# Kernel optimization log

Measured on AMD Instinct MI355X. Metric: run time of the kernel, lower is better.

The kernel has to match this reference:

```python
import jax, jax.numpy as jnp
import numpy as np

EPS_BN = 1e-5
NUM_DIR = 32


def _bn(x, g, b, m, v):
    # x: (B, C, N); inference-mode batchnorm over channel dim
    return (x - m[None, :, None]) / jnp.sqrt(v[None, :, None] + EPS_BN) * g[None, :, None] + b[None, :, None]


def _conv1(w, x):
    # 1x1 Conv1d: w (O, C), x (B, C, N) -> (B, O, N)
    return jnp.einsum('oc,bcn->bon', w, x)


def _knn_max(fc, idx):
    # fc: (B, C, N), idx: (B, N, K) -> max over gathered neighbors, (B, C, N)
    B = fc.shape[0]
    f_bnc = jnp.transpose(fc, (0, 2, 1))                      # (B, N, C)
    g = f_bnc[jnp.arange(B)[:, None, None], idx]              # (B, N, K, C)
    return jnp.transpose(g.max(axis=2), (0, 2, 1))            # (B, C, N)


def setup_inputs() -> dict:
    key = jax.random.key(0)
    ks = jax.random.split(key, 24)
    B, C, N, K = 4, 128, 8192, 16
    H = C // 2
    inp = {
        'f': jax.random.normal(ks[0], (B, C, N), jnp.float32),
        'dp': jax.random.normal(ks[1], (B, 3, N, K), jnp.float32),
        'qidx': jax.random.randint(ks[2], (B, N, K), 0, N),
        # DirectionalEncoding params
        'dir_vectors': jax.random.normal(ks[3], (NUM_DIR, 3), jnp.float32),
        'de_w1': jax.random.normal(ks[4], (H, NUM_DIR), jnp.float32) * 0.1,
        'de_bn_g': jax.random.uniform(ks[5], (H,), jnp.float32, 0.5, 1.5),
        'de_bn_b': jax.random.normal(ks[6], (H,), jnp.float32) * 0.1,
        'de_bn_m': jax.random.normal(ks[7], (H,), jnp.float32) * 0.1,
        'de_bn_v': jax.random.uniform(ks[8], (H,), jnp.float32, 0.5, 1.5),
        'de_w2': jax.random.normal(ks[9], (C, H), jnp.float32) * 0.1,
        'de_b2': jax.random.normal(ks[10], (C,), jnp.float32) * 0.1,
        # LPFMA params
        'l_w1': jax.random.normal(ks[11], (C, C), jnp.float32) * 0.05,
        'l_b1': jax.random.normal(ks[12], (C,), jnp.float32) * 0.05,
        'l_w2': jax.random.normal(ks[13], (C, C), jnp.float32) * 0.05,
        'l_b2': jax.random.normal(ks[14], (C,), jnp.float32) * 0.05,
        'l_w3': jax.random.normal(ks[15], (C, C), jnp.float32) * 0.05,
        'l_b3': jax.random.normal(ks[16], (C,), jnp.float32) * 0.05,
        'l_bn_g': jax.random.uniform(ks[17], (C,), jnp.float32, 0.5, 1.5),
        'l_bn_b': jax.random.normal(ks[18], (C,), jnp.float32) * 0.1,
        'l_bn_m': jax.random.normal(ks[19], (C,), jnp.float32) * 0.1,
        'l_bn_v': jax.random.uniform(ks[20], (C,), jnp.float32, 0.5, 1.5),
        # Mlp params (hid = 2*C)
        'm_w1': jax.random.normal(ks[21], (2 * C, C), jnp.float32) * 0.05,
        'm_bn_g': jnp.ones((2 * C,), jnp.float32),
        'm_bn_b': jnp.zeros((2 * C,), jnp.float32),
        'm_bn_m': jnp.zeros((2 * C,), jnp.float32),
        'm_bn_v': jnp.ones((2 * C,), jnp.float32),
        'm_w2': jax.random.normal(ks[22], (C, 2 * C), jnp.float32) * 0.05,
    }
    return inp


def _forward(f, dp, qidx, dir_vectors, de_w1, de_bn_g, de_bn_b, de_bn_m, de_bn_v,
             de_w2, de_b2, l_w1, l_b1, l_w2, l_b2, l_w3, l_b3,
             l_bn_g, l_bn_b, l_bn_m, l_bn_v, m_w1, m_bn_g, m_bn_b, m_bn_m, m_bn_v, m_w2):
    B, C3, N, K = dp.shape
    # --- DirectionalEncoding ---
    dp_norm = dp / jnp.maximum(jnp.linalg.norm(dp, axis=1, keepdims=True), 1e-12)
    vec_norm = dir_vectors / jnp.maximum(jnp.linalg.norm(dir_vectors, axis=1, keepdims=True), 1e-12)
    theta = jnp.einsum('md,bdnk->bmnk', vec_norm, dp_norm)    # (B, 32, N, K)
    theta_max = theta.max(axis=-1)                             # (B, 32, N)
    h = _bn(_conv1(de_w1, theta_max), de_bn_g, de_bn_b, de_bn_m, de_bn_v)
    h = jax.nn.gelu(h, approximate=False)
    pe = _conv1(de_w2, h) + de_b2[None, :, None]               # (B, C, N)
    # --- LPFMA ---
    f1 = _conv1(l_w1, f) + l_b1[None, :, None]
    f2 = _conv1(l_w2, f) + l_b2[None, :, None]
    f3 = _conv1(l_w3, f) + l_b3[None, :, None]
    agg1 = _knn_max(f1, qidx)
    agg2 = _knn_max(f2, qidx) + f2
    f_agg = _bn(agg1 + agg2 + f3, l_bn_g, l_bn_b, l_bn_m, l_bn_v)
    # bn_after=False -> bn0/bn1 are Identity
    f = f + (f_agg + pe)
    # --- Mlp ---
    h2 = _bn(_conv1(m_w1, f), m_bn_g, m_bn_b, m_bn_m, m_bn_v)
    h2 = jax.nn.gelu(h2, approximate=False)
    f = f + _conv1(m_w2, h2)
    return f


def reference(f, dp, qidx, dir_vectors, de_w1, de_bn_g, de_bn_b, de_bn_m, de_bn_v,
              de_w2, de_b2, l_w1, l_b1, l_w2, l_b2, l_w3, l_b3,
              l_bn_g, l_bn_b, l_bn_m, l_bn_v, m_w1, m_bn_g, m_bn_b, m_bn_m, m_bn_v, m_w2):
    return _forward(f, dp, qidx, dir_vectors, de_w1, de_bn_g, de_bn_b, de_bn_m, de_bn_v,
                    de_w2, de_b2, l_w1, l_b1, l_w2, l_b2, l_w3, l_b3,
                    l_bn_g, l_bn_b, l_bn_m, l_bn_v, m_w1, m_bn_g, m_bn_b, m_bn_m, m_bn_v, m_w2)
```

## Files before the change

kernel.cpp:

```cpp
#include <hip/hip_runtime.h>
#include <hip/hip_bf16.h>
#include <cstdint>
#include <cstddef>

#define BB 4
#define CC 128
#define NN 8192
#define KK 16
#define HH 64
#define MM 32
#define C2 256

typedef __attribute__((ext_vector_type(8))) short bf16x8;
typedef __attribute__((ext_vector_type(4))) float f32x4;
typedef unsigned short u16x2v __attribute__((ext_vector_type(2)));
typedef unsigned int u32x2 __attribute__((ext_vector_type(2)));
typedef unsigned int u32x4 __attribute__((ext_vector_type(4)));

__device__ __forceinline__ unsigned short f2bf(float f){
    unsigned int x = __float_as_uint(f);
    x += 0x7fffu + ((x >> 16) & 1u);
    return (unsigned short)(x >> 16);
}
__device__ __forceinline__ unsigned int pk2(float a, float b){
    return (unsigned int)f2bf(a) | ((unsigned int)f2bf(b) << 16);
}
__device__ __forceinline__ float lo16(unsigned int u){ return __uint_as_float(u << 16); }
__device__ __forceinline__ float hi16(unsigned int u){ return __uint_as_float(u & 0xffff0000u); }
__device__ __forceinline__ float gelu(float a){
    return 0.5f*a*(1.0f+erff(a*0.7071067811865475f));
}
__device__ __forceinline__ unsigned int bf2key(unsigned int v){
    unsigned int neg = (v >> 15) & 0x10001u;
    return v ^ (0x80008000u | neg * 0x7FFFu);
}
__device__ __forceinline__ unsigned int key2bf(unsigned int k){
    unsigned int pos = (~k >> 15) & 0x10001u;
    return k ^ (0x80008000u | pos * 0x7FFFu);
}
__device__ __forceinline__ unsigned int pkmax(unsigned int a, unsigned int b){
    u16x2v r = __builtin_elementwise_max(__builtin_bit_cast(u16x2v, a),
                                         __builtin_bit_cast(u16x2v, b));
    return __builtin_bit_cast(unsigned int, r);
}
__device__ __forceinline__ void xcd_remap(int bid, int& b, int& tile){
    int xcd = bid & 7;
    b = xcd >> 1;
    tile = (bid >> 3) * 2 + (xcd & 1);
}

__global__ __launch_bounds__(256) void k_pe(
    const float* __restrict__ dp, const float* __restrict__ dirs,
    const float* __restrict__ w1,
    const float* __restrict__ bng, const float* __restrict__ bnb,
    const float* __restrict__ bnm, const float* __restrict__ bnv,
    const float* __restrict__ w2, const float* __restrict__ b2,
    unsigned short* __restrict__ pe)
{
    __shared__ float s_dx[MM], s_dy[MM], s_dz[MM];
    __shared__ alignas(16) float dnx[64*16], dny[64*16], dnz[64*16];
    __shared__ alignas(16) unsigned short th[64*32];
    __shared__ alignas(16) unsigned short ws1[64*32];
    __shared__ alignas(16) unsigned short hs[64*64];
    __shared__ alignas(16) unsigned short ws2[128*64];
    __shared__ float s_sc[HH], s_sh[HH], s_b2[CC];

    const int tid = threadIdx.x;
    int b, tile; xcd_remap(blockIdx.x, b, tile);
    const int n0 = tile * 64;

    if (tid < MM){
        float x=dirs[tid*3+0], y=dirs[tid*3+1], z=dirs[tid*3+2];
        float inv = 1.0f / fmaxf(sqrtf(x*x+y*y+z*z), 1e-12f);
        s_dx[tid]=x*inv; s_dy[tid]=y*inv; s_dz[tid]=z*inv;
    }
    #pragma unroll
    for (int p=0;p<2;p++){
        int id = tid + p*256;
        int row = id >> 3, c4 = (id & 7)*4;
        float4 w = *(const float4*)(w1 + row*MM + c4);
        int off = row*64 + ((c4*2) ^ ((row&3)<<4));
        uint2 v; v.x = pk2(w.x,w.y); v.y = pk2(w.z,w.w);
        *(uint2*)((char*)ws1 + off) = v;
    }
    #pragma unroll
    for (int p=0;p<8;p++){
        int id = tid + p*256;
        int row = id >> 4, c4 = (id & 15)*4;
        float4 w = *(const float4*)(w2 + row*HH + c4);
        int off = row*128 + ((c4*2) ^ ((row&7)<<4));
        uint2 v; v.x = pk2(w.x,w.y); v.y = pk2(w.z,w.w);
        *(uint2*)((char*)ws2 + off) = v;
    }
    if (tid < HH){
        float sc = bng[tid] / sqrtf(bnv[tid] + 1e-5f);
        s_sc[tid]=sc; s_sh[tid]=bnb[tid]-bnm[tid]*sc;
    }
    if (tid >= 64 && tid < 192) s_b2[tid-64] = b2[tid-64];

    {
        const size_t cstride = (size_t)NN*KK;
        const float* base = dp + (size_t)b*3*cstride + (size_t)n0*KK + tid*4;
        float4 X = *(const float4*)(base);
        float4 Y = *(const float4*)(base + cstride);
        float4 Z = *(const float4*)(base + 2*cstride);
        float i0 = 1.0f/fmaxf(sqrtf(X.x*X.x+Y.x*Y.x+Z.x*Z.x),1e-12f);
        float i1 = 1.0f/fmaxf(sqrtf(X.y*X.y+Y.y*Y.y+Z.y*Z.y),1e-12f);
        float i2 = 1.0f/fmaxf(sqrtf(X.z*X.z+Y.z*Y.z+Z.z*Z.z),1e-12f);
        float i3 = 1.0f/fmaxf(sqrtf(X.w*X.w+Y.w*Y.w+Z.w*Z.w),1e-12f);
        float4 xn = {X.x*i0, X.y*i1, X.z*i2, X.w*i3};
        float4 yn = {Y.x*i0, Y.y*i1, Y.z*i2, Y.w*i3};
        float4 zn = {Z.x*i0, Z.y*i1, Z.z*i2, Z.w*i3};
        const int np = tid >> 2;
        const int off = np*64 + (((tid&3)*16) ^ ((np&3)<<4));
        *(float4*)((char*)dnx + off) = xn;
        *(float4*)((char*)dny + off) = yn;
        *(float4*)((char*)dnz + off) = zn;
    }
    __syncthreads();

    {
        const int np = tid & 63, dg = tid >> 6;
        float vx[8], vy[8], vz[8];
        #pragma unroll
        for (int d=0;d<8;d++){ vx[d]=s_dx[dg*8+d]; vy[d]=s_dy[dg*8+d]; vz[d]=s_dz[dg*8+d]; }
        float tm[8];
        #pragma unroll
        for (int d=0;d<8;d++) tm[d] = -2.0f;
        #pragma unroll
        for (int g=0;g<4;g++){
            int off = np*64 + ((g*16) ^ ((np&3)<<4));
            float4 x4 = *(const float4*)((const char*)dnx + off);
            float4 y4 = *(const float4*)((const char*)dny + off);
            float4 z4 = *(const float4*)((const char*)dnz + off);
            const float xs[4]={x4.x,x4.y,x4.z,x4.w}, ys[4]={y4.x,y4.y,y4.z,y4.w},
                        zs[4]={z4.x,z4.y,z4.z,z4.w};
            #pragma unroll
            for (int q=0;q<4;q++)
                #pragma unroll
                for (int d=0;d<8;d++)
                    tm[d] = fmaxf(tm[d], vx[d]*xs[q]+vy[d]*ys[q]+vz[d]*zs[q]);
        }
        uint4 t4; t4.x=pk2(tm[0],tm[1]); t4.y=pk2(tm[2],tm[3]);
        t4.z=pk2(tm[4],tm[5]); t4.w=pk2(tm[6],tm[7]);
        int off = np*64 + ((dg*16) ^ ((np&3)<<4));
        *(uint4*)((char*)th + off) = t4;
    }
    __syncthreads();

    const int wid = tid >> 6, lane = tid & 63;
    const int lr = lane & 15, lg = lane >> 4;

    {
        const int arow = wid*16 + lr;
        bf16x8 afr = *(const bf16x8*)((const char*)ws1 + arow*64 + ((lg*16) ^ ((arow&3)<<4)));
        f32x4 hacc[4];
        #pragma unroll
        for (int nf=0;nf<4;nf++){
            int pt = nf*16 + lr;
            bf16x8 bfr = *(const bf16x8*)((const char*)th + pt*64 + ((lg*16) ^ ((pt&3)<<4)));
            f32x4 z = {0.f,0.f,0.f,0.f};
            hacc[nf] = __builtin_amdgcn_mfma_f32_16x16x32_bf16(afr, bfr, z, 0,0,0);
        }
        #pragma unroll
        for (int nf=0;nf<4;nf++){
            int ch0 = wid*16 + lg*4;
            int pt = nf*16 + lr;
            float g0 = gelu(hacc[nf].x*s_sc[ch0+0] + s_sh[ch0+0]);
            float g1 = gelu(hacc[nf].y*s_sc[ch0+1] + s_sh[ch0+1]);
            float g2 = gelu(hacc[nf].z*s_sc[ch0+2] + s_sh[ch0+2]);
            float g3 = gelu(hacc[nf].w*s_sc[ch0+3] + s_sh[ch0+3]);
            uint2 v; v.x = pk2(g0,g1); v.y = pk2(g2,g3);
            *(uint2*)((char*)hs + pt*128 + ((ch0*2) ^ ((pt&7)<<4))) = v;
        }
    }
    __syncthreads();

    {
        f32x4 pacc[2][4];
        #pragma unroll
        for (int mi=0;mi<2;mi++)
            #pragma unroll
            for (int nf=0;nf<4;nf++) pacc[mi][nf] = (f32x4){0.f,0.f,0.f,0.f};
        #pragma unroll
        for (int ks=0;ks<2;ks++){
            bf16x8 a[2], x[4];
            #pragma unroll
            for (int mi=0;mi<2;mi++){
                int row = (wid*2+mi)*16 + lr;
                a[mi] = *(const bf16x8*)((const char*)ws2 + row*128 + ((ks*64 + lg*16) ^ ((row&7)<<4)));
            }
            #pragma unroll
            for (int nf=0;nf<4;nf++){
                int pt = nf*16 + lr;
                x[nf] = *(const bf16x8*)((const char*)hs + pt*128 + ((ks*64 + lg*16) ^ ((pt&7)<<4)));
            }
            #pragma unroll
            for (int mi=0;mi<2;mi++)
                #pragma unroll
                for (int nf=0;nf<4;nf++)
                    pacc[mi][nf] = __builtin_amdgcn_mfma_f32_16x16x32_bf16(a[mi], x[nf], pacc[mi][nf], 0,0,0);
        }
        #pragma unroll
        for (int mi=0;mi<2;mi++){
            #pragma unroll
            for (int nf=0;nf<4;nf++){
                int ch0 = (wid*2+mi)*16 + lg*4;
                int pt = nf*16 + lr;
                u32x2 v;
                v.x = pk2(pacc[mi][nf].x + s_b2[ch0+0], pacc[mi][nf].y + s_b2[ch0+1]);
                v.y = pk2(pacc[mi][nf].z + s_b2[ch0+2], pacc[mi][nf].w + s_b2[ch0+3]);
                __builtin_nontemporal_store(v, (u32x2*)(pe + (size_t)(b*NN + n0 + pt)*CC + ch0));
            }
        }
    }
}

__global__ __launch_bounds__(256) void k_lin3(
    const float* __restrict__ f,
    const float* __restrict__ w1g, const float* __restrict__ b1g,
    const float* __restrict__ w2g, const float* __restrict__ b2g,
    const float* __restrict__ w3g, const float* __restrict__ b3g,
    unsigned short* __restrict__ t1, unsigned short* __restrict__ t2,
    unsigned short* __restrict__ f3t, unsigned short* __restrict__ ft)
{
    __shared__ alignas(16) unsigned short Xs[64*128];
    __shared__ alignas(16) unsigned short Ws[128*128];
    __shared__ float s_bias[128];
    const int tid = threadIdx.x;
    int b, tile;
    xcd_remap(blockIdx.x, b, tile);
    const int n0 = tile * 64;

    {
        const int j = (tid & 15) * 4;
        #pragma unroll
        for (int p = 0; p < 2; ++p){
            const int cb = ((tid >> 4) + p*16) * 4;
            const float* src = f + ((size_t)b*CC + cb)*NN + n0 + j;
            float4 r0 = *(const float4*)(src);
            float4 r1 = *(const float4*)(src + NN);
            float4 r2 = *(const float4*)(src + 2*(size_t)NN);
            float4 r3 = *(const float4*)(src + 3*(size_t)NN);
            const float rr[4][4] = {{r0.x,r1.x,r2.x,r3.x},{r0.y,r1.y,r2.y,r3.y},
                                    {r0.z,r1.z,r2.z,r3.z},{r0.w,r1.w,r2.w,r3.w}};
            #pragma unroll
            for (int i=0;i<4;i++){
                int n = j + i;
                int off = n*256 + ((cb*2) ^ ((n&7)<<4));
                uint2 v; v.x = pk2(rr[i][0], rr[i][1]); v.y = pk2(rr[i][2], rr[i][3]);
                *(uint2*)((char*)Xs + off) = v;
            }
        }
    }
    __syncthreads();
    #pragma unroll
    for (int q=0;q<4;q++){
        int idx = tid + q*256;
        int n = idx >> 4, c8 = (idx & 15)*8;
        int off = n*256 + ((c8*2) ^ ((n&7)<<4));
        u32x4 v = *(const u32x4*)((const char*)Xs + off);
        __builtin_nontemporal_store(v, (u32x4*)(ft + (size_t)(b*NN + n0 + n)*CC + c8));
    }

    const int wid = tid >> 6, lane = tid & 63;
    const int lr = lane & 15, lg = lane >> 4;
    const int o0 = (wid >> 1) * 64;
    const int nl0 = (wid & 1) * 32;

    for (int mat = 0; mat < 3; ++mat){
        const float* Wg = (mat==0)? w1g : (mat==1)? w2g : w3g;
        const float* Bg = (mat==0)? b1g : (mat==1)? b2g : b3g;
        __syncthreads();
        #pragma unroll 4
        for (int p = 0; p < 16; ++p){
            int o = (tid >> 5) + p*8;
            int c4 = (tid & 31) * 4;
            float4 w = *(const float4*)(Wg + (size_t)o*CC + c4);
            int off = o*256 + ((c4*2) ^ ((o&7)<<4));
            uint2 v; v.x = pk2(w.x, w.y); v.y = pk2(w.z, w.w);
            *(uint2*)((char*)Ws + off) = v;
        }
        if (tid < 128) s_bias[tid] = Bg[tid];
        __syncthreads();

        f32x4 acc[4][2];
        #pragma unroll
        for (int fi=0;fi<4;fi++){
            int o = o0 + fi*16 + lg*4;
            f32x4 bi = {s_bias[o], s_bias[o+1], s_bias[o+2], s_bias[o+3]};
            acc[fi][0] = bi; acc[fi][1] = bi;
        }
        #pragma unroll
        for (int kk=0; kk<4; ++kk){
            const int kb = kk*64 + lg*16;
            bf16x8 a[4], x[2];
            #pragma unroll
            for (int fi=0;fi<4;fi++){
                int row = o0 + fi*16 + lr;
                a[fi] = *(const bf16x8*)((const char*)Ws + row*256 + (kb ^ ((row&7)<<4)));
            }
            #pragma unroll
            for (int fj=0;fj<2;fj++){
                int nr = nl0 + fj*16 + lr;
                x[fj] = *(const bf16x8*)((const char*)Xs + nr*256 + (kb ^ ((nr&7)<<4)));
            }
            #pragma unroll
            for (int fi=0;fi<4;fi++)
                #pragma unroll
                for (int fj=0;fj<2;fj++)
                    acc[fi][fj] = __builtin_amdgcn_mfma_f32_16x16x32_bf16(a[fi], x[fj], acc[fi][fj], 0,0,0);
        }
        #pragma unroll
        for (int fi=0;fi<4;fi++){
            #pragma unroll
            for (int fj=0;fj<2;fj++){
                int o = o0 + fi*16 + lg*4;
                int n = n0 + nl0 + fj*16 + lr;
                if (mat == 2){
                    u32x2 u;
                    u.x = pk2(acc[fi][fj].x, acc[fi][fj].y);
                    u.y = pk2(acc[fi][fj].z, acc[fi][fj].w);
                    __builtin_nontemporal_store(u, (u32x2*)(f3t + (size_t)(b*NN + n)*CC + o));
                } else {
                    unsigned short* dst = (mat==0)? t1 : t2;
                    uint2 kv;
                    kv.x = bf2key(pk2(acc[fi][fj].x, acc[fi][fj].y));
                    kv.y = bf2key(pk2(acc[fi][fj].z, acc[fi][fj].w));
                    *(uint2*)(dst + (size_t)(b*NN + n)*CC + o) = kv;
                }
            }
        }
    }
}

__global__ __launch_bounds__(256) void k_gather(
    const int* __restrict__ qidx,
    const unsigned short* __restrict__ t1,
    const unsigned short* __restrict__ t2,
    unsigned short* __restrict__ agg1,
    unsigned short* __restrict__ agg2)
{
    const int tid = threadIdx.x;
    const int lane = tid & 63, wrp = tid >> 6;
    const int bid = blockIdx.x;
    const int xcd = bid & 7;
    const int b = xcd >> 1, half = xcd & 1;
    const int tile = bid >> 3;
    const int p0 = b*NN + tile*8 + wrp*2;
    const unsigned short* tab = half ? t2 : t1;
    const unsigned int* gb = (const unsigned int*)(tab + (size_t)b*NN*CC) + lane;
    const int prow = __builtin_amdgcn_readfirstlane(p0);
    const int* i0 = qidx + (size_t)prow*KK;

    unsigned int m0 = 0, m1 = 0;
    #pragma unroll
    for (int k=0;k<KK;k++){
        int j0 = i0[k];
        int j1 = i0[KK + k];
        unsigned int g0 = gb[(size_t)j0*64];
        unsigned int g1 = gb[(size_t)j1*64];
        m0 = pkmax(m0, g0);
        m1 = pkmax(m1, g1);
    }
    unsigned int r0 = key2bf(m0), r1 = key2bf(m1);
    float a00 = lo16(r0), a01 = hi16(r0);
    float a10 = lo16(r1), a11 = hi16(r1);
    if (half){
        unsigned int s0 = key2bf(((const unsigned int*)(tab + (size_t)p0*CC))[lane]);
        unsigned int s1 = key2bf(((const unsigned int*)(tab + (size_t)(p0+1)*CC))[lane]);
        a00 += lo16(s0); a01 += hi16(s0);
        a10 += lo16(s1); a11 += hi16(s1);
    }
    unsigned short* aout = half ? agg2 : agg1;
    __builtin_nontemporal_store(pk2(a00,a01), (unsigned int*)(aout + (size_t)p0*CC) + lane);
    __builtin_nontemporal_store(pk2(a10,a11), (unsigned int*)(aout + (size_t)(p0+1)*CC) + lane);
}

__global__ __launch_bounds__(256) void k_h2o(
    const unsigned short* __restrict__ agg1,
    const unsigned short* __restrict__ agg2,
    const unsigned short* __restrict__ ft,
    const unsigned short* __restrict__ f3t,
    const unsigned short* __restrict__ pe,
    const float* __restrict__ l_bng, const float* __restrict__ l_bnb,
    const float* __restrict__ l_bnm, const float* __restrict__ l_bnv,
    const float* __restrict__ w1g,
    const float* __restrict__ bng, const float* __restrict__ bnb,
    const float* __restrict__ bnm, const float* __restrict__ bnv,
    const float* __restrict__ w2g,
    float* __restrict__ out)
{
    __shared__ alignas(16) unsigned short Xs[64*128];
    __shared__ alignas(16) unsigned short Ws[128*128];
    __shared__ alignas(16) unsigned short Hs[64*128];
    __shared__ float s_lsc[128], s_lsh[128];
    __shared__ float s_msc[256], s_msh[256];
    const int tid = threadIdx.x;
    int b, tile;
    xcd_remap(blockIdx.x, b, tile);
    const int n0 = tile * 64;

    if (tid < 128){
        float sc = l_bng[tid] / sqrtf(l_bnv[tid] + 1e-5f);
        s_lsc[tid] = sc; s_lsh[tid] = l_bnb[tid] - l_bnm[tid]*sc;
    }
    {
        float sc = bng[tid] / sqrtf(bnv[tid] + 1e-5f);
        s_msc[tid] = sc; s_msh[tid] = bnb[tid] - bnm[tid]*sc;
    }
    __syncthreads();

    #pragma unroll
    for (int q=0;q<4;q++){
        int idx = tid + q*256;
        int n = idx >> 4, c8 = (idx & 15)*8;
        size_t base = (size_t)(b*NN + n0 + n)*CC + c8;
        u32x4 a1 = __builtin_nontemporal_load((const u32x4*)(agg1 + base));
        u32x4 a2 = __builtin_nontemporal_load((const u32x4*)(agg2 + base));
        u32x4 fv = __builtin_nontemporal_load((const u32x4*)(ft   + base));
        u32x4 f3 = __builtin_nontemporal_load((const u32x4*)(f3t  + base));
        u32x4 pv = __builtin_nontemporal_load((const u32x4*)(pe   + base));
        u32x4 r;
        #pragma unroll
        for (int e=0;e<4;e++){
            int c = c8 + e*2;
            float slo = lo16(a1[e]) + lo16(a2[e]) + lo16(f3[e]);
            float shi = hi16(a1[e]) + hi16(a2[e]) + hi16(f3[e]);
            float vlo = lo16(fv[e]) + slo*s_lsc[c]   + s_lsh[c]   + lo16(pv[e]);
            float vhi = hi16(fv[e]) + shi*s_lsc[c+1] + s_lsh[c+1] + hi16(pv[e]);
            r[e] = pk2(vlo, vhi);
        }
        int off = n*256 + ((c8*2) ^ ((n&7)<<4));
        *(u32x4*)((char*)Xs + off) = r;
    }

    const int lane = tid & 63, wrp = tid >> 6;
    const int lr = lane & 15, lg = lane >> 4;
    const int o0 = (wrp >> 1) * 64;
    const int nl0 = (wrp & 1) * 32;

    f32x4 oacc[4][2];
    #pragma unroll
    for (int fi=0;fi<4;fi++){ oacc[fi][0]=(f32x4){0,0,0,0}; oacc[fi][1]=(f32x4){0,0,0,0}; }

    for (int jh = 0; jh < 2; ++jh){
        __syncthreads();
        {
            const float* Wg = w1g + (size_t)jh*128*CC;
            #pragma unroll 4
            for (int p = 0; p < 16; ++p){
                int o = (tid >> 5) + p*8;
                int c4 = (tid & 31) * 4;
                float4 w = *(const float4*)(Wg + (size_t)o*CC + c4);
                int off = o*256 + ((c4*2) ^ ((o&7)<<4));
                uint2 v; v.x = pk2(w.x, w.y); v.y = pk2(w.z, w.w);
                *(uint2*)((char*)Ws + off) = v;
            }
        }
        __syncthreads();
        {
            f32x4 hacc[4][2];
            #pragma unroll
            for (int fi=0;fi<4;fi++){ hacc[fi][0]=(f32x4){0,0,0,0}; hacc[fi][1]=(f32x4){0,0,0,0}; }
            #pragma unroll
            for (int kk=0; kk<4; ++kk){
                const int kb = kk*64 + lg*16;
                bf16x8 a[4], x[2];
                #pragma unroll
                for (int fi=0;fi<4;fi++){
                    int row = o0 + fi*16 + lr;
                    a[fi] = *(const bf16x8*)((const char*)Ws + row*256 + (kb ^ ((row&7)<<4)));
                }
                #pragma unroll
                for (int fj=0;fj<2;fj++){
                    int nr = nl0 + fj*16 + lr;
                    x[fj] = *(const bf16x8*)((const char*)Xs + nr*256 + (kb ^ ((nr&7)<<4)));
                }
                #pragma unroll
                for (int fi=0;fi<4;fi++)
                    #pragma unroll
                    for (int fj=0;fj<2;fj++)
                        hacc[fi][fj] = __builtin_amdgcn_mfma_f32_16x16x32_bf16(a[fi], x[fj], hacc[fi][fj], 0,0,0);
            }
            #pragma unroll
            for (int fi=0;fi<4;fi++){
                #pragma unroll
                for (int fj=0;fj<2;fj++){
                    int o = o0 + fi*16 + lg*4;
                    int jo = jh*128 + o;
                    int nl = nl0 + fj*16 + lr;
                    float v0 = gelu(hacc[fi][fj].x*s_msc[jo+0] + s_msh[jo+0]);
                    float v1 = gelu(hacc[fi][fj].y*s_msc[jo+1] + s_msh[jo+1]);
                    float v2 = gelu(hacc[fi][fj].z*s_msc[jo+2] + s_msh[jo+2]);
                    float v3 = gelu(hacc[fi][fj].w*s_msc[jo+3] + s_msh[jo+3]);
                    u32x2 v; v.x = pk2(v0,v1); v.y = pk2(v2,v3);
                    *(u32x2*)((char*)Hs + nl*256 + ((o*2) ^ ((nl&7)<<4))) = v;
                }
            }
        }
        __syncthreads();
        {
            #pragma unroll 4
            for (int p = 0; p < 16; ++p){
                int o = (tid >> 5) + p*8;
                int c4 = (tid & 31) * 4;
                float4 w = *(const float4*)(w2g + (size_t)o*C2 + jh*128 + c4);
                int off = o*256 + ((c4*2) ^ ((o&7)<<4));
                uint2 v; v.x = pk2(w.x, w.y); v.y = pk2(w.z, w.w);
                *(uint2*)((char*)Ws + off) = v;
            }
        }
        __syncthreads();
        #pragma unroll
        for (int kk=0; kk<4; ++kk){
            const int kb = kk*64 + lg*16;
            bf16x8 a[4], x[2];
            #pragma unroll
            for (int fi=0;fi<4;fi++){
                int row = o0 + fi*16 + lr;
                a[fi] = *(const bf16x8*)((const char*)Ws + row*256 + (kb ^ ((row&7)<<4)));
            }
            #pragma unroll
            for (int fj=0;fj<2;fj++){
                int nr = nl0 + fj*16 + lr;
                x[fj] = *(const bf16x8*)((const char*)Hs + nr*256 + (kb ^ ((nr&7)<<4)));
            }
            #pragma unroll
            for (int fi=0;fi<4;fi++)
                #pragma unroll
                for (int fj=0;fj<2;fj++)
                    oacc[fi][fj] = __builtin_amdgcn_mfma_f32_16x16x32_bf16(a[fi], x[fj], oacc[fi][fj], 0,0,0);
        }
    }
    #pragma unroll
    for (int fi=0;fi<4;fi++){
        #pragma unroll
        for (int fj=0;fj<2;fj++){
            int o = o0 + fi*16 + lg*4;
            int nl = nl0 + fj*16 + lr;
            int n = n0 + nl;
            u32x2 fm = *(const u32x2*)((const char*)Xs + nl*256 + ((o*2) ^ ((nl&7)<<4)));
            float* op = out + ((size_t)b*CC + o)*NN + n;
            op[0*(size_t)NN] = lo16(fm.x) + oacc[fi][fj].x;
            op[1*(size_t)NN] = hi16(fm.x) + oacc[fi][fj].y;
            op[2*(size_t)NN] = lo16(fm.y) + oacc[fi][fj].z;
            op[3*(size_t)NN] = hi16(fm.y) + oacc[fi][fj].w;
        }
    }
}

extern "C" void kernel_launch(void* const* d_in, const int* in_sizes, int n_in,
                              void* d_out, int out_size, void* d_ws, size_t ws_size,
                              hipStream_t stream)
{
    const float* f      = (const float*)d_in[0];
    const float* dp     = (const float*)d_in[1];
    const int*   qidx   = (const int*)  d_in[2];
    const float* dirs   = (const float*)d_in[3];
    const float* de_w1  = (const float*)d_in[4];
    const float* de_bng = (const float*)d_in[5];
    const float* de_bnb = (const float*)d_in[6];
    const float* de_bnm = (const float*)d_in[7];
    const float* de_bnv = (const float*)d_in[8];
    const float* de_w2  = (const float*)d_in[9];
    const float* de_b2  = (const float*)d_in[10];
    const float* l_w1   = (const float*)d_in[11];
    const float* l_b1   = (const float*)d_in[12];
    const float* l_w2   = (const float*)d_in[13];
    const float* l_b2   = (const float*)d_in[14];
    const float* l_w3   = (const float*)d_in[15];
    const float* l_b3   = (const float*)d_in[16];
    const float* l_bng  = (const float*)d_in[17];
    const float* l_bnb  = (const float*)d_in[18];
    const float* l_bnm  = (const float*)d_in[19];
    const float* l_bnv  = (const float*)d_in[20];
    const float* m_w1   = (const float*)d_in[21];
    const float* m_bng  = (const float*)d_in[22];
    const float* m_bnb  = (const float*)d_in[23];
    const float* m_bnm  = (const float*)d_in[24];
    const float* m_bnv  = (const float*)d_in[25];
    const float* m_w2   = (const float*)d_in[26];

    char* ws = (char*)d_ws;
    unsigned short* t1    = (unsigned short*)(ws + 0);
    unsigned short* t2    = (unsigned short*)(ws + 8388608);
    unsigned short* ft    = (unsigned short*)(ws + 16777216);
    unsigned short* f3t   = (unsigned short*)(ws + 25165824);
    unsigned short* pe    = (unsigned short*)(ws + 33554432);
    unsigned short* agg1  = (unsigned short*)(ws + 41943040);
    unsigned short* agg2  = (unsigned short*)(ws + 50331648);

    k_pe<<<dim3(512), dim3(256), 0, stream>>>(dp, dirs, de_w1, de_bng, de_bnb, de_bnm, de_bnv,
                                              de_w2, de_b2, pe);
    k_lin3<<<dim3(512), dim3(256), 0, stream>>>(f, l_w1, l_b1, l_w2, l_b2, l_w3, l_b3,
                                                t1, t2, f3t, ft);
    k_gather<<<dim3(8192), dim3(256), 0, stream>>>(qidx, t1, t2, agg1, agg2);
    k_h2o<<<dim3(512), dim3(256), 0, stream>>>(agg1, agg2, ft, f3t, pe,
                                               l_bng, l_bnb, l_bnm, l_bnv,
                                               m_w1, m_bng, m_bnb, m_bnm, m_bnv,
                                               m_w2, (float*)d_out);
}
```

Baseline: 77.87 us.

## Fuse PE and linear kernels, precombine residual base, pre-convert weights once

Result: faster. 66.60 us (-14.5%).

```diff
diff --git a/kernel.cpp b/kernel.cpp
--- a/kernel.cpp
+++ b/kernel.cpp
@@ -49,21 +49,56 @@
     tile = (bid >> 3) * 2 + (xcd & 1);
 }
 
-__global__ __launch_bounds__(256) void k_pe(
+__global__ __launch_bounds__(256) void k_wcv(
+    const float* __restrict__ lw1, const float* __restrict__ lw2,
+    const float* __restrict__ lw3, const float* __restrict__ mw1,
+    const float* __restrict__ mw2, unsigned short* __restrict__ wb)
+{
+    const int tid = threadIdx.x;
+    const int img = blockIdx.x >> 4;
+    const int chunk = blockIdx.x & 15;
+    const int o = chunk*8 + (tid >> 5);
+    const int c4 = (tid & 31)*4;
+    const float* src;
+    if (img < 3)      src = (img==0? lw1 : img==1? lw2 : lw3) + (size_t)o*128 + c4;
+    else if (img < 5) src = mw1 + ((size_t)(img-3)*128 + o)*128 + c4;
+    else              src = mw2 + (size_t)o*256 + (size_t)(img-5)*128 + c4;
+    float4 w = *(const float4*)src;
+    uint2 v; v.x = pk2(w.x, w.y); v.y = pk2(w.z, w.w);
+    *(uint2*)((char*)wb + (size_t)img*32768 + o*256 + ((c4*2) ^ ((o&7)<<4))) = v;
+}
+
+__global__ __launch_bounds__(256) void k_linpe(
+    const float* __restrict__ f,
     const float* __restrict__ dp, const float* __restrict__ dirs,
-    const float* __restrict__ w1,
-    const float* __restrict__ bng, const float* __restrict__ bnb,
-    const float* __restrict__ bnm, const float* __restrict__ bnv,
-    const float* __restrict__ w2, const float* __restrict__ b2,
-    unsigned short* __restrict__ pe)
+    const float* __restrict__ de_w1,
+    const float* __restrict__ de_bng, const float* __restrict__ de_bnb,
+    const float* __restrict__ de_bnm, const float* __restrict__ de_bnv,
+    const float* __restrict__ de_w2, const float* __restrict__ de_b2,
+    const unsigned short* __restrict__ wb,
+    const float* __restrict__ b1g, const float* __restrict__ b2g,
+    const float* __restrict__ b3g,
+    const float* __restrict__ l_bng, const float* __restrict__ l_bnb,
+    const float* __restrict__ l_bnm, const float* __restrict__ l_bnv,
+    unsigned short* __restrict__ t1, unsigned short* __restrict__ t2,
+    unsigned short* __restrict__ baseb)
 {
+    __shared__ alignas(16) char sraw[45056];
+    __shared__ alignas(16) unsigned short Xs[64*128];
+    __shared__ alignas(16) unsigned short peL[64*128];
     __shared__ float s_dx[MM], s_dy[MM], s_dz[MM];
-    __shared__ alignas(16) float dnx[64*16], dny[64*16], dnz[64*16];
-    __shared__ alignas(16) unsigned short th[64*32];
-    __shared__ alignas(16) unsigned short ws1[64*32];
-    __shared__ alignas(16) unsigned short hs[64*64];
-    __shared__ alignas(16) unsigned short ws2[128*64];
     __shared__ float s_sc[HH], s_sh[HH], s_b2[CC];
+    __shared__ float s_lsc[CC], s_lsh[CC];
+    __shared__ float s_bias[128];
+
+    float* dnx = (float*)(sraw + 0);
+    float* dny = (float*)(sraw + 4096);
+    float* dnz = (float*)(sraw + 8192);
+    unsigned short* th  = (unsigned short*)(sraw + 12288);
+    unsigned short* ws1 = (unsigned short*)(sraw + 16384);
+    unsigned short* ws2 = (unsigned short*)(sraw + 20480);
+    unsigned short* hs  = (unsigned short*)(sraw + 36864);
+    unsigned short* Ws  = (unsigned short*)(sraw + 0);
 
     const int tid = threadIdx.x;
     int b, tile; xcd_remap(blockIdx.x, b, tile);
@@ -78,7 +113,7 @@
     for (int p=0;p<2;p++){
         int id = tid + p*256;
         int row = id >> 3, c4 = (id & 7)*4;
-        float4 w = *(const float4*)(w1 + row*MM + c4);
+        float4 w = *(const float4*)(de_w1 + row*MM + c4);
         int off = row*64 + ((c4*2) ^ ((row&3)<<4));
         uint2 v; v.x = pk2(w.x,w.y); v.y = pk2(w.z,w.w);
         *(uint2*)((char*)ws1 + off) = v;
@@ -87,17 +122,41 @@
     for (int p=0;p<8;p++){
         int id = tid + p*256;
         int row = id >> 4, c4 = (id & 15)*4;
-        float4 w = *(const float4*)(w2 + row*HH + c4);
+        float4 w = *(const float4*)(de_w2 + row*HH + c4);
         int off = row*128 + ((c4*2) ^ ((row&7)<<4));
         uint2 v; v.x = pk2(w.x,w.y); v.y = pk2(w.z,w.w);
         *(uint2*)((char*)ws2 + off) = v;
     }
     if (tid < HH){
-        float sc = bng[tid] / sqrtf(bnv[tid] + 1e-5f);
-        s_sc[tid]=sc; s_sh[tid]=bnb[tid]-bnm[tid]*sc;
-    }
-    if (tid >= 64 && tid < 192) s_b2[tid-64] = b2[tid-64];
-
+        float sc = de_bng[tid] / sqrtf(de_bnv[tid] + 1e-5f);
+        s_sc[tid]=sc; s_sh[tid]=de_bnb[tid]-de_bnm[tid]*sc;
+    }
+    if (tid >= 64 && tid < 192) s_b2[tid-64] = de_b2[tid-64];
+    if (tid < CC){
+        float sc = l_bng[tid] / sqrtf(l_bnv[tid] + 1e-5f);
+        s_lsc[tid] = sc; s_lsh[tid] = l_bnb[tid] - l_bnm[tid]*sc;
+    }
+    {
+        const int j = (tid & 15) * 4;
+        #pragma unroll
+        for (int p = 0; p < 2; ++p){
+            const int cb = ((tid >> 4) + p*16) * 4;
+            const float* src = f + ((size_t)b*CC + cb)*NN + n0 + j;
+            float4 r0 = *(const float4*)(src);
+            float4 r1 = *(const float4*)(src + NN);
+            float4 r2 = *(const float4*)(src + 2*(size_t)NN);
+            float4 r3 = *(const float4*)(src + 3*(size_t)NN);
+            const float rr[4][4] = {{r0.x,r1.x,r2.x,r3.x},{r0.y,r1.y,r2.y,r3.y},
+                                    {r0.z,r1.z,r2.z,r3.z},{r0.w,r1.w,r2.w,r3.w}};
+            #pragma unroll
+            for (int i=0;i<4;i++){
+                int n = j + i;
+                int off = n*256 + ((cb*2) ^ ((n&7)<<4));
+                uint2 v; v.x = pk2(rr[i][0], rr[i][1]); v.y = pk2(rr[i][2], rr[i][3]);
+                *(uint2*)((char*)Xs + off) = v;
+            }
+        }
+    }
     {
         const size_t cstride = (size_t)NN*KK;
         const float* base = dp + (size_t)b*3*cstride + (size_t)n0*KK + tid*4;
@@ -207,79 +266,27 @@
             for (int nf=0;nf<4;nf++){
                 int ch0 = (wid*2+mi)*16 + lg*4;
                 int pt = nf*16 + lr;
-                u32x2 v;
+                uint2 v;
                 v.x = pk2(pacc[mi][nf].x + s_b2[ch0+0], pacc[mi][nf].y + s_b2[ch0+1]);
                 v.y = pk2(pacc[mi][nf].z + s_b2[ch0+2], pacc[mi][nf].w + s_b2[ch0+3]);
-                __builtin_nontemporal_store(v, (u32x2*)(pe + (size_t)(b*NN + n0 + pt)*CC + ch0));
-            }
-        }
-    }
-}
-
-__global__ __launch_bounds__(256) void k_lin3(
-    const float* __restrict__ f,
-    const float* __restrict__ w1g, const float* __restrict__ b1g,
-    const float* __restrict__ w2g, const float* __restrict__ b2g,
-    const float* __restrict__ w3g, const float* __restrict__ b3g,
-    unsigned short* __restrict__ t1, unsigned short* __restrict__ t2,
-    unsigned short* __restrict__ f3t, unsigned short* __restrict__ ft)
-{
-    __shared__ alignas(16) unsigned short Xs[64*128];
-    __shared__ alignas(16) unsigned short Ws[128*128];
-    __shared__ float s_bias[128];
-    const int tid = threadIdx.x;
-    int b, tile;
-    xcd_remap(blockIdx.x, b, tile);
-    const int n0 = tile * 64;
-
-    {
-        const int j = (tid & 15) * 4;
-        #pragma unroll
-        for (int p = 0; p < 2; ++p){
-            const int cb = ((tid >> 4) + p*16) * 4;
-            const float* src = f + ((size_t)b*CC + cb)*NN + n0 + j;
-            float4 r0 = *(const float4*)(src);
-            float4 r1 = *(const float4*)(src + NN);
-            float4 r2 = *(const float4*)(src + 2*(size_t)NN);
-            float4 r3 = *(const float4*)(src + 3*(size_t)NN);
-            const float rr[4][4] = {{r0.x,r1.x,r2.x,r3.x},{r0.y,r1.y,r2.y,r3.y},
-                                    {r0.z,r1.z,r2.z,r3.z},{r0.w,r1.w,r2.w,r3.w}};
-            #pragma unroll
-            for (int i=0;i<4;i++){
-                int n = j + i;
-                int off = n*256 + ((cb*2) ^ ((n&7)<<4));
-                uint2 v; v.x = pk2(rr[i][0], rr[i][1]); v.y = pk2(rr[i][2], rr[i][3]);
-                *(uint2*)((char*)Xs + off) = v;
-            }
-        }
-    }
-    __syncthreads();
-    #pragma unroll
-    for (int q=0;q<4;q++){
-        int idx = tid + q*256;
-        int n = idx >> 4, c8 = (idx & 15)*8;
-        int off = n*256 + ((c8*2) ^ ((n&7)<<4));
-        u32x4 v = *(const u32x4*)((const char*)Xs + off);
-        __builtin_nontemporal_store(v, (u32x4*)(ft + (size_t)(b*NN + n0 + n)*CC + c8));
-    }
-
-    const int wid = tid >> 6, lane = tid & 63;
-    const int lr = lane & 15, lg = lane >> 4;
+                *(uint2*)((char*)peL + pt*256 + ((ch0*2) ^ ((pt&7)<<4))) = v;
+            }
+        }
+    }
+
     const int o0 = (wid >> 1) * 64;
     const int nl0 = (wid & 1) * 32;
 
     for (int mat = 0; mat < 3; ++mat){
-        const float* Wg = (mat==0)? w1g : (mat==1)? w2g : w3g;
         const float* Bg = (mat==0)? b1g : (mat==1)? b2g : b3g;
         __syncthreads();
-        #pragma unroll 4
-        for (int p = 0; p < 16; ++p){
-            int o = (tid >> 5) + p*8;
-            int c4 = (tid & 31) * 4;
-            float4 w = *(const float4*)(Wg + (size_t)o*CC + c4);
-            int off = o*256 + ((c4*2) ^ ((o&7)<<4));
-            uint2 v; v.x = pk2(w.x, w.y); v.y = pk2(w.z, w.w);
-            *(uint2*)((char*)Ws + off) = v;
+        {
+            const char* img = (const char*)wb + (size_t)mat*32768;
+            #pragma unroll
+            for (int p=0;p<8;p++){
+                int off = tid*16 + p*4096;
+                *(u32x4*)((char*)Ws + off) = *(const u32x4*)(img + off);
+            }
         }
         if (tid < 128) s_bias[tid] = Bg[tid];
         __syncthreads();
@@ -316,12 +323,17 @@
             #pragma unroll
             for (int fj=0;fj<2;fj++){
                 int o = o0 + fi*16 + lg*4;
-                int n = n0 + nl0 + fj*16 + lr;
+                int nl = nl0 + fj*16 + lr;
+                int n = n0 + nl;
                 if (mat == 2){
-                    u32x2 u;
-                    u.x = pk2(acc[fi][fj].x, acc[fi][fj].y);
-                    u.y = pk2(acc[fi][fj].z, acc[fi][fj].w);
-                    __builtin_nontemporal_store(u, (u32x2*)(f3t + (size_t)(b*NN + n)*CC + o));
+                    u32x2 fm = *(const u32x2*)((const char*)Xs  + nl*256 + ((o*2) ^ ((nl&7)<<4)));
+                    u32x2 pv = *(const u32x2*)((const char*)peL + nl*256 + ((o*2) ^ ((nl&7)<<4)));
+                    float v0 = lo16(fm.x) + acc[fi][fj].x*s_lsc[o+0] + s_lsh[o+0] + lo16(pv.x);
+                    float v1 = hi16(fm.x) + acc[fi][fj].y*s_lsc[o+1] + s_lsh[o+1] + hi16(pv.x);
+                    float v2 = lo16(fm.y) + acc[fi][fj].z*s_lsc[o+2] + s_lsh[o+2] + lo16(pv.y);
+                    float v3 = hi16(fm.y) + acc[fi][fj].w*s_lsc[o+3] + s_lsh[o+3] + hi16(pv.y);
+                    u32x2 r; r.x = pk2(v0,v1); r.y = pk2(v2,v3);
+                    __builtin_nontemporal_store(r, (u32x2*)(baseb + (size_t)(b*NN + n)*CC + o));
                 } else {
                     unsigned short* dst = (mat==0)? t1 : t2;
                     uint2 kv;
@@ -380,31 +392,24 @@
 __global__ __launch_bounds__(256) void k_h2o(
     const unsigned short* __restrict__ agg1,
     const unsigned short* __restrict__ agg2,
-    const unsigned short* __restrict__ ft,
-    const unsigned short* __restrict__ f3t,
-    const unsigned short* __restrict__ pe,
-    const float* __restrict__ l_bng, const float* __restrict__ l_bnb,
-    const float* __restrict__ l_bnm, const float* __restrict__ l_bnv,
-    const float* __restrict__ w1g,
+    const unsigned short* __restrict__ baseb,
+    const float* __restrict__ l_bng, const float* __restrict__ l_bnv,
+    const unsigned short* __restrict__ wb,
     const float* __restrict__ bng, const float* __restrict__ bnb,
     const float* __restrict__ bnm, const float* __restrict__ bnv,
-    const float* __restrict__ w2g,
     float* __restrict__ out)
 {
     __shared__ alignas(16) unsigned short Xs[64*128];
     __shared__ alignas(16) unsigned short Ws[128*128];
     __shared__ alignas(16) unsigned short Hs[64*128];
-    __shared__ float s_lsc[128], s_lsh[128];
+    __shared__ float s_lsc[128];
     __shared__ float s_msc[256], s_msh[256];
     const int tid = threadIdx.x;
     int b, tile;
     xcd_remap(blockIdx.x, b, tile);
     const int n0 = tile * 64;
 
-    if (tid < 128){
-        float sc = l_bng[tid] / sqrtf(l_bnv[tid] + 1e-5f);
-        s_lsc[tid] = sc; s_lsh[tid] = l_bnb[tid] - l_bnm[tid]*sc;
-    }
+    if (tid < 128) s_lsc[tid] = l_bng[tid] / sqrtf(l_bnv[tid] + 1e-5f);
     {
         float sc = bng[tid] / sqrtf(bnv[tid] + 1e-5f);
         s_msc[tid] = sc; s_msh[tid] = bnb[tid] - bnm[tid]*sc;
@@ -418,17 +423,13 @@
         size_t base = (size_t)(b*NN + n0 + n)*CC + c8;
         u32x4 a1 = __builtin_nontemporal_load((const u32x4*)(agg1 + base));
         u32x4 a2 = __builtin_nontemporal_load((const u32x4*)(agg2 + base));
-        u32x4 fv = __builtin_nontemporal_load((const u32x4*)(ft   + base));
-        u32x4 f3 = __builtin_nontemporal_load((const u32x4*)(f3t  + base));
-        u32x4 pv = __builtin_nontemporal_load((const u32x4*)(pe   + base));
+        u32x4 bv = __builtin_nontemporal_load((const u32x4*)(baseb + base));
         u32x4 r;
         #pragma unroll
         for (int e=0;e<4;e++){
             int c = c8 + e*2;
-            float slo = lo16(a1[e]) + lo16(a2[e]) + lo16(f3[e]);
-            float shi = hi16(a1[e]) + hi16(a2[e]) + hi16(f3[e]);
-            float vlo = lo16(fv[e]) + slo*s_lsc[c]   + s_lsh[c]   + lo16(pv[e]);
-            float vhi = hi16(fv[e]) + shi*s_lsc[c+1] + s_lsh[c+1] + hi16(pv[e]);
+            float vlo = lo16(bv[e]) + (lo16(a1[e]) + lo16(a2[e]))*s_lsc[c];
+            float vhi = hi16(bv[e]) + (hi16(a1[e]) + hi16(a2[e]))*s_lsc[c+1];
             r[e] = pk2(vlo, vhi);
         }
         int off = n*256 + ((c8*2) ^ ((n&7)<<4));
@@ -447,15 +448,11 @@
     for (int jh = 0; jh < 2; ++jh){
         __syncthreads();
         {
-            const float* Wg = w1g + (size_t)jh*128*CC;
-            #pragma unroll 4
-            for (int p = 0; p < 16; ++p){
-                int o = (tid >> 5) + p*8;
-                int c4 = (tid & 31) * 4;
-                float4 w = *(const float4*)(Wg + (size_t)o*CC + c4);
-                int off = o*256 + ((c4*2) ^ ((o&7)<<4));
-                uint2 v; v.x = pk2(w.x, w.y); v.y = pk2(w.z, w.w);
-                *(uint2*)((char*)Ws + off) = v;
+            const char* img = (const char*)wb + (size_t)(3+jh)*32768;
+            #pragma unroll
+            for (int p=0;p<8;p++){
+                int off = tid*16 + p*4096;
+                *(u32x4*)((char*)Ws + off) = *(const u32x4*)(img + off);
             }
         }
         __syncthreads();
@@ -501,14 +498,11 @@
         }
         __syncthreads();
         {
-            #pragma unroll 4
-            for (int p = 0; p < 16; ++p){
-                int o = (tid >> 5) + p*8;
-                int c4 = (tid & 31) * 4;
-                float4 w = *(const float4*)(w2g + (size_t)o*C2 + jh*128 + c4);
-                int off = o*256 + ((c4*2) ^ ((o&7)<<4));
-                uint2 v; v.x = pk2(w.x, w.y); v.y = pk2(w.z, w.w);
-                *(uint2*)((char*)Ws + off) = v;
+            const char* img = (const char*)wb + (size_t)(5+jh)*32768;
+            #pragma unroll
+            for (int p=0;p<8;p++){
+                int off = tid*16 + p*4096;
+                *(u32x4*)((char*)Ws + off) = *(const u32x4*)(img + off);
             }
         }
         __syncthreads();
@@ -585,19 +579,21 @@
     char* ws = (char*)d_ws;
     unsigned short* t1    = (unsigned short*)(ws + 0);
     unsigned short* t2    = (unsigned short*)(ws + 8388608);
-    unsigned short* ft    = (unsigned short*)(ws + 16777216);
-    unsigned short* f3t   = (unsigned short*)(ws + 25165824);
-    unsigned short* pe    = (unsigned short*)(ws + 33554432);
-    unsigned short* agg1  = (unsigned short*)(ws + 41943040);
-    unsigned short* agg2  = (unsigned short*)(ws + 50331648);
-
-    k_pe<<<dim3(512), dim3(256), 0, stream>>>(dp, dirs, de_w1, de_bng, de_bnb, de_bnm, de_bnv,
-                                              de_w2, de_b2, pe);
-    k_lin3<<<dim3(512), dim3(256), 0, stream>>>(f, l_w1, l_b1, l_w2, l_b2, l_w3, l_b3,
-                                                t1, t2, f3t, ft);
+    unsigned short* baseb = (unsigned short*)(ws + 16777216);
+    unsigned short* agg1  = (unsigned short*)(ws + 25165824);
+    unsigned short* agg2  = (unsigned short*)(ws + 33554432);
+    unsigned short* wb    = (unsigned short*)(ws + 41943040);
+
+    k_wcv<<<dim3(112), dim3(256), 0, stream>>>(l_w1, l_w2, l_w3, m_w1, m_w2, wb);
+    k_linpe<<<dim3(512), dim3(256), 0, stream>>>(f, dp, dirs,
+                                                 de_w1, de_bng, de_bnb, de_bnm, de_bnv,
+                                                 de_w2, de_b2, wb,
+                                                 l_b1, l_b2, l_b3,
+                                                 l_bng, l_bnb, l_bnm, l_bnv,
+                                                 t1, t2, baseb);
     k_gather<<<dim3(8192), dim3(256), 0, stream>>>(qidx, t1, t2, agg1, agg2);
-    k_h2o<<<dim3(512), dim3(256), 0, stream>>>(agg1, agg2, ft, f3t, pe,
-                                               l_bng, l_bnb, l_bnm, l_bnv,
-                                               m_w1, m_bng, m_bnb, m_bnm, m_bnv,
-                                               m_w2, (float*)d_out);
-}
+    k_h2o<<<dim3(512), dim3(256), 0, stream>>>(agg1, agg2, baseb,
+                                               l_bng, l_bnv, wb,
+                                               m_bng, m_bnb, m_bnm, m_bnv,
+                                               (float*)d_out);
+}
```
